# Performance work log

Hardware: AMD Instinct MI355X
Metric: run time of the kernel (lower is better)

The kernel has to match this reference:

```python
import jax, jax.numpy as jnp
import numpy as np

B, S, C = 512, 512, 32
H, L, P = 512, 2, 96


def _init(key, shape, scale=0.1):
    return jax.random.uniform(key, shape, jnp.float32, -scale, scale)


def setup_inputs() -> dict:
    key = jax.random.key(0)
    ks = jax.random.split(key, 10)
    return {
        "x": jax.random.normal(ks[0], (B, S, C), jnp.float32),
        "Wi0": _init(ks[1], (3 * H, C)),
        "Wh0": _init(ks[2], (3 * H, H)),
        "b0": _init(ks[3], (3 * H,)),
        "Wi1": _init(ks[4], (3 * H, H)),
        "Wh1": _init(ks[5], (3 * H, H)),
        "b1": _init(ks[6], (3 * H,)),
        "Wp": _init(ks[7], (P * C, H)),
        "bp": _init(ks[8], (P * C,)),
    }


def _gru_cell(xt, h, Wi, Wh, b):
    # xt: (B, in), h: (B, H). Gates stacked [r; z; n].
    gi = xt @ Wi.T + b                       # (B, 3H), fused input-side GEMM
    gir, giz, gin = jnp.split(gi, 3, axis=-1)
    Whr, Whz, Whn = jnp.split(Wh, 3, axis=0)
    r = jax.nn.sigmoid(gir + h @ Whr.T)
    z = jax.nn.sigmoid(giz + h @ Whz.T)
    # NOTE: source parses as (r * h) @ W_hn.T (reset BEFORE matmul)
    n = jnp.tanh(gin + (r * h) @ Whn.T)
    return (1.0 - z) * n + z * h


def reference(x, Wi0, Wh0, b0, Wi1, Wh1, b1, Wp, bp):
    batch = x.shape[0]
    h0 = jnp.zeros((batch, H), x.dtype)
    h1 = jnp.zeros((batch, H), x.dtype)

    def step(carry, xt):
        h0, h1 = carry
        h0 = _gru_cell(xt, h0, Wi0, Wh0, b0)
        h1 = _gru_cell(h0, h1, Wi1, Wh1, b1)
        return (h0, h1), None

    xs = jnp.swapaxes(x, 0, 1)               # (S, B, C)
    (h0, h1), _ = jax.lax.scan(step, (h0, h1), xs)
    pred = h1 @ Wp.T + bp                    # (B, P*C)
    return pred.reshape(batch, P, C)
```

## Files before the change

kernel.cpp:

```cpp
#include <hip/hip_runtime.h>
#include <cstdint>
#include <cstddef>


typedef _Float16 f16;
typedef _Float16 half8 __attribute__((ext_vector_type(8)));
typedef float f32x4 __attribute__((ext_vector_type(4)));
typedef unsigned long long u64;

#define NT 256
#define NBLK 256
#define SEQ 512
#define SC 2048.0f
#define INV_SC (1.0f / 2048.0f)
#define MFMA16(a, b, c) __builtin_amdgcn_mfma_f32_16x16x32_f16(a, b, c, 0, 0, 0)

constexpr size_t OFF_WH0H = 0;
constexpr size_t OFF_WH0L = 1572864;
constexpr size_t OFF_WI1H = 3145728;
constexpr size_t OFF_WI1L = 4718592;
constexpr size_t OFF_WH1H = 6291456;
constexpr size_t OFF_WH1L = 7864320;
constexpr size_t OFF_WPH  = 9437184;
constexpr size_t OFF_WI0H = 12582912;
constexpr size_t OFF_WI0L = 12681216;
constexpr size_t OFF_H0H  = 12779520;
constexpr size_t OFF_H0L  = 13303808;
constexpr size_t OFF_H1H0 = 13828096;
constexpr size_t OFF_H1L0 = 14352384;
constexpr size_t OFF_H1H1 = 14876672;
constexpr size_t OFF_H1L1 = 15400960;
constexpr size_t OFF_RH0  = 15925248;
constexpr size_t OFF_RH1  = 16449536;
constexpr size_t OFF_Z0   = 16973824;
constexpr size_t OFF_Z1   = 17498112;
constexpr size_t OFF_GIN  = 18022400;
constexpr size_t OFF_BAR  = 19070976;

constexpr int LO_BA   = 0;
constexpr int LO_BB   = 65536;
constexpr int LO_WXA  = 98304;
constexpr int LO_WXB  = 103424;
constexpr int LO_STG0 = 106496;
constexpr int LO_STG1 = 126976;
constexpr int LDS_BYTES = 147456;

__device__ __forceinline__ float sigm(float v) { return 1.f / (1.f + __expf(-v)); }
__device__ __forceinline__ float tanh_f(float v) { float e = __expf(2.f * v); return 1.f - 2.f / (e + 1.f); }
__device__ __forceinline__ void split2(float v, f16& hi, f16& lo) {
  f16 h = (f16)v; hi = h; lo = (f16)((v - (float)h) * SC);
}
__device__ __forceinline__ void st16(f16* p, f16 v) {
  union { f16 f; unsigned short u; } cv; cv.f = v;
  __hip_atomic_store((unsigned short*)p, cv.u, __ATOMIC_RELAXED, __HIP_MEMORY_SCOPE_AGENT);
}
__device__ __forceinline__ void st32(float* p, float v) {
  __hip_atomic_store(p, v, __ATOMIC_RELAXED, __HIP_MEMORY_SCOPE_AGENT);
}
__device__ __forceinline__ float ld16f(const f16* p) {
  unsigned short u = __hip_atomic_load((const unsigned short*)p, __ATOMIC_RELAXED, __HIP_MEMORY_SCOPE_AGENT);
  union { unsigned short u; f16 f; } cv; cv.u = u; return (float)cv.f;
}
__device__ __forceinline__ float ld32f(const float* p) {
  return __hip_atomic_load(p, __ATOMIC_RELAXED, __HIP_MEMORY_SCOPE_AGENT);
}
__device__ __forceinline__ void ld16a(const f16* p, uint4& v) {
  const u64* q = (const u64*)p;
  u64 a = __hip_atomic_load(q,     __ATOMIC_RELAXED, __HIP_MEMORY_SCOPE_AGENT);
  u64 b = __hip_atomic_load(q + 1, __ATOMIC_RELAXED, __HIP_MEMORY_SCOPE_AGENT);
  v.x = (unsigned)a; v.y = (unsigned)(a >> 32);
  v.z = (unsigned)b; v.w = (unsigned)(b >> 32);
}

__device__ __forceinline__ void ldB512(char* dst, int row0, const f16* __restrict__ src,
                                       int srcRow0, int nrows, int tid) {
  for (int idx = tid; idx < nrows * 64; idx += NT) {
    int r = idx >> 6, g = idx & 63;
    uint4 v = *(const uint4*)(src + (size_t)(srcRow0 + r) * 512 + g * 8);
    int row = row0 + r;
    *(uint4*)(dst + ((row * 1024 + g * 16) ^ ((row & 7) << 4))) = v;
  }
}
__device__ __forceinline__ void ldWX(char* wx, int row0, const f16* __restrict__ src,
                                     int srcRow0, int nrows, int tid) {
  for (int idx = tid; idx < nrows * 4; idx += NT) {
    int r = idx >> 2, g = idx & 3;
    uint4 v = *(const uint4*)(src + (size_t)(srcRow0 + r) * 32 + g * 8);
    *(uint4*)(wx + (row0 + r) * 80 + g * 16) = v;
  }
}

template<int FM>
__device__ __forceinline__ void runA(const f16* __restrict__ src, int m0, char* lds,
                                     int wm, int rowH, int rowL,
                                     int tid, int lr, int lkb,
                                     f32x4 (&am)[FM], f32x4 (&ac)[FM]) {
  char* S0 = lds + LO_STG0; char* S1 = lds + LO_STG1;
  const char* BA = lds + LO_BA;
  uint4 r0[4], r1[4], r2[4], r3[4];
  auto ld = [&](int c, uint4 (&v)[4]) {
#pragma unroll
    for (int j = 0; j < 4; ++j) { int idx = tid + j * NT; int r = idx >> 2, g = idx & 3;
      ld16a(src + (size_t)(m0 + r) * 512 + c * 32 + g * 8, v[j]); } };
  auto st = [&](char* S, uint4 (&v)[4]) {
#pragma unroll
    for (int j = 0; j < 4; ++j) { int idx = tid + j * NT; int r = idx >> 2, g = idx & 3;
      *(uint4*)(S + r * 80 + g * 16) = v[j]; } };
  auto mm = [&](const char* S, int c) {
    int rh = rowH + lr, rl = rowL + lr;
    half8 bh = *(const half8*)(BA + ((rh * 1024 + c * 64 + lkb) ^ ((rh & 7) << 4)));
    half8 bl = *(const half8*)(BA + ((rl * 1024 + c * 64 + lkb) ^ ((rl & 7) << 4)));
#pragma unroll
    for (int fm = 0; fm < FM; ++fm) {
      half8 a = *(const half8*)(S + (wm + fm * 16 + lr) * 80 + lkb);
      am[fm] = MFMA16(a, bh, am[fm]); ac[fm] = MFMA16(a, bl, ac[fm]); } };
  ld(0, r0); ld(1, r1); ld(2, r2); ld(3, r3);
  st(S0, r0);
  __syncthreads();
#pragma unroll 1
  for (int c0 = 0; c0 < 16; c0 += 4) {
    if (c0 + 4 < 16) ld(c0 + 4, r0);
    mm(S0, c0);     st(S1, r1); __syncthreads();
    if (c0 + 5 < 16) ld(c0 + 5, r1);
    mm(S1, c0 + 1); st(S0, r2); __syncthreads();
    if (c0 + 6 < 16) ld(c0 + 6, r2);
    mm(S0, c0 + 2); st(S1, r3); __syncthreads();
    if (c0 + 7 < 16) ld(c0 + 7, r3);
    mm(S1, c0 + 3); st(S0, r0); __syncthreads();
  }
}

__device__ __forceinline__ void runA1(const f16* __restrict__ s0p, const f16* __restrict__ s1p,
                                      int m0, char* lds, int wm,
                                      int tid, int lr, int lkb,
                                      f32x4 (&am)[4], f32x4 (&ac)[4]) {
  char* S0 = lds + LO_STG0; char* S1 = lds + LO_STG1;
  const char* BA = lds + LO_BA;
  uint4 r0[4], r1[4], r2[4], r3[4];
  auto ld = [&](int c, uint4 (&v)[4]) {
    const f16* s = (c < 16) ? s0p : s1p; int k0 = (c & 15) * 32;
#pragma unroll
    for (int j = 0; j < 4; ++j) { int idx = tid + j * NT; int r = idx >> 2, g = idx & 3;
      ld16a(s + (size_t)(m0 + r) * 512 + k0 + g * 8, v[j]); } };
  auto st = [&](char* S, uint4 (&v)[4]) {
#pragma unroll
    for (int j = 0; j < 4; ++j) { int idx = tid + j * NT; int r = idx >> 2, g = idx & 3;
      *(uint4*)(S + r * 80 + g * 16) = v[j]; } };
  auto mm = [&](const char* S, int c) {
    int rb = (c < 16) ? 0 : 32; int kB = (c & 15) * 64;
    int rh = rb + lr, rl = rb + 16 + lr;
    half8 bh = *(const half8*)(BA + ((rh * 1024 + kB + lkb) ^ ((rh & 7) << 4)));
    half8 bl = *(const half8*)(BA + ((rl * 1024 + kB + lkb) ^ ((rl & 7) << 4)));
#pragma unroll
    for (int fm = 0; fm < 4; ++fm) {
      half8 a = *(const half8*)(S + (wm + fm * 16 + lr) * 80 + lkb);
      am[fm] = MFMA16(a, bh, am[fm]); ac[fm] = MFMA16(a, bl, ac[fm]); } };
  ld(0, r0); ld(1, r1); ld(2, r2); ld(3, r3);
  st(S0, r0);
  __syncthreads();
#pragma unroll 1
  for (int c0 = 0; c0 < 32; c0 += 4) {
    if (c0 + 4 < 32) ld(c0 + 4, r0);
    mm(S0, c0);     st(S1, r1); __syncthreads();
    if (c0 + 5 < 32) ld(c0 + 5, r1);
    mm(S1, c0 + 1); st(S0, r2); __syncthreads();
    if (c0 + 6 < 32) ld(c0 + 6, r2);
    mm(S0, c0 + 2); st(S1, r3); __syncthreads();
    if (c0 + 7 < 32) ld(c0 + 7, r3);
    mm(S1, c0 + 3); st(S0, r0); __syncthreads();
  }
}

template<int FM>
__device__ __forceinline__ void runB(const f16* __restrict__ src, int m0, char* lds,
                                     int wm, int tid, int lr, int lkb,
                                     f32x4 (&am)[FM], f32x4 (&ac)[FM]) {
  char* S0 = lds + LO_STG0; char* S1 = lds + LO_STG1;
  const char* BB = lds + LO_BB;
  uint4 r0[4], r1[4], r2[4], r3[4];
  auto ld = [&](int c, uint4 (&v)[4]) {
#pragma unroll
    for (int j = 0; j < 4; ++j) { int idx = tid + j * NT; int r = idx >> 3, g = idx & 7;
      ld16a(src + (size_t)(m0 + r) * 512 + c * 64 + g * 8, v[j]); } };
  auto st = [&](char* S, uint4 (&v)[4]) {
#pragma unroll
    for (int j = 0; j < 4; ++j) { int idx = tid + j * NT; int r = idx >> 3, g = idx & 7;
      *(uint4*)(S + r * 144 + g * 16) = v[j]; } };
  auto mm = [&](const char* S, int c) {
#pragma unroll
    for (int ki = 0; ki < 2; ++ki) {
      int rh = lr, rl = 16 + lr;
      half8 bh = *(const half8*)(BB + ((rh * 1024 + c * 128 + ki * 64 + lkb) ^ ((rh & 7) << 4)));
      half8 bl = *(const half8*)(BB + ((rl * 1024 + c * 128 + ki * 64 + lkb) ^ ((rl & 7) << 4)));
#pragma unroll
      for (int fm = 0; fm < FM; ++fm) {
        half8 a = *(const half8*)(S + (wm + fm * 16 + lr) * 144 + ki * 64 + lkb);
        am[fm] = MFMA16(a, bh, am[fm]); ac[fm] = MFMA16(a, bl, ac[fm]); } } };
  ld(0, r0); ld(1, r1); ld(2, r2); ld(3, r3);
  st(S0, r0);
  __syncthreads();
#pragma unroll 1
  for (int c0 = 0; c0 < 8; c0 += 4) {
    if (c0 + 4 < 8) ld(c0 + 4, r0);
    mm(S0, c0);     st(S1, r1); __syncthreads();
    if (c0 + 5 < 8) ld(c0 + 5, r1);
    mm(S1, c0 + 1); st(S0, r2); __syncthreads();
    if (c0 + 6 < 8) ld(c0 + 6, r2);
    mm(S0, c0 + 2); st(S1, r3); __syncthreads();
    if (c0 + 7 < 8) ld(c0 + 7, r3);
    mm(S1, c0 + 3); st(S0, r0); __syncthreads();
  }
}

template<int FM>
__device__ __forceinline__ void mmX(const char* S0, const char* S1, const char* wx,
                                    int wm, int rowH, int rowL, int lr, int lkb,
                                    f32x4 (&am)[FM], f32x4 (&ac)[FM]) {
  half8 bh = *(const half8*)(wx + (rowH + lr) * 80 + lkb);
  half8 bl = *(const half8*)(wx + (rowL + lr) * 80 + lkb);
#pragma unroll
  for (int fm = 0; fm < FM; ++fm) {
    half8 axh = *(const half8*)(S0 + (wm + fm * 16 + lr) * 80 + lkb);
    half8 axl = *(const half8*)(S1 + (wm + fm * 16 + lr) * 80 + lkb);
    am[fm] = MFMA16(axh, bh, am[fm]);
    ac[fm] = MFMA16(axh, bl, ac[fm]);
    ac[fm] = MFMA16(axl, bh, ac[fm]);
  }
}

__device__ __forceinline__ void gbar(unsigned* bar, int bid, int tid, unsigned lg) {
  __syncthreads();
  if (bid == 0) {
    if (tid == 0) {
      __threadfence();
    } else {
      while (__hip_atomic_load(bar + tid * 16, __ATOMIC_RELAXED, __HIP_MEMORY_SCOPE_AGENT) < lg)
        __builtin_amdgcn_s_sleep(1);
    }
    __syncthreads();
    if (tid < 16)
      __hip_atomic_store(bar + 4096 + tid * 16, lg, __ATOMIC_RELAXED, __HIP_MEMORY_SCOPE_AGENT);
  } else if (tid == 0) {
    __threadfence();
    __hip_atomic_store(bar + bid * 16, lg, __ATOMIC_RELAXED, __HIP_MEMORY_SCOPE_AGENT);
  }
  if (tid == 0) {
    while (__hip_atomic_load(bar + 4096 + (bid & 15) * 16, __ATOMIC_RELAXED, __HIP_MEMORY_SCOPE_AGENT) < lg)
      __builtin_amdgcn_s_sleep(1);
  }
  __syncthreads();
}

__global__ void gru_setup(const float* __restrict__ Wi0, const float* __restrict__ Wh0,
                          const float* __restrict__ Wi1, const float* __restrict__ Wh1,
                          const float* __restrict__ Wp, char* __restrict__ ws) {
  size_t t = (size_t)blockIdx.x * blockDim.x + threadIdx.x;
  size_t st = (size_t)gridDim.x * blockDim.x;
  f16* wh0h = (f16*)(ws + OFF_WH0H); f16* wh0l = (f16*)(ws + OFF_WH0L);
  f16* wi1h = (f16*)(ws + OFF_WI1H); f16* wi1l = (f16*)(ws + OFF_WI1L);
  f16* wh1h = (f16*)(ws + OFF_WH1H); f16* wh1l = (f16*)(ws + OFF_WH1L);
  f16* wph  = (f16*)(ws + OFF_WPH);
  f16* wi0h = (f16*)(ws + OFF_WI0H); f16* wi0l = (f16*)(ws + OFF_WI0L);
  for (size_t j = t; j < (size_t)1536 * 512; j += st) {
    split2(Wh0[j], wh0h[j], wh0l[j]);
    split2(Wi1[j], wi1h[j], wi1l[j]);
    split2(Wh1[j], wh1h[j], wh1l[j]);
  }
  for (size_t j = t; j < (size_t)3072 * 512; j += st) wph[j] = (f16)Wp[j];
  for (size_t j = t; j < (size_t)1536 * 32; j += st) split2(Wi0[j], wi0h[j], wi0l[j]);
  f16* mir = (f16*)(ws + OFF_H0H);
  for (size_t j = t; j < (size_t)512 * 512 * 10; j += st) mir[j] = (f16)0.f;
  unsigned* bar = (unsigned*)(ws + OFF_BAR);
  for (size_t j = t; j < 8192; j += st) bar[j] = 0u;
}

__global__ __launch_bounds__(NT, 1) void gru_main(
    const float* __restrict__ x, const float* __restrict__ b0, const float* __restrict__ b1,
    const float* __restrict__ bp, float* __restrict__ out, char* __restrict__ ws)
{
  extern __shared__ char lds[];

  const f16* WH0Hp = (const f16*)(ws + OFF_WH0H); const f16* WH0Lp = (const f16*)(ws + OFF_WH0L);
  const f16* WI1Hp = (const f16*)(ws + OFF_WI1H); const f16* WI1Lp = (const f16*)(ws + OFF_WI1L);
  const f16* WH1Hp = (const f16*)(ws + OFF_WH1H); const f16* WH1Lp = (const f16*)(ws + OFF_WH1L);
  const f16* WPHp  = (const f16*)(ws + OFF_WPH);
  const f16* WI0Hp = (const f16*)(ws + OFF_WI0H); const f16* WI0Lp = (const f16*)(ws + OFF_WI0L);
  f16* H0H = (f16*)(ws + OFF_H0H);
  f16* H0L = (f16*)(ws + OFF_H0L);
  f16* RH0 = (f16*)(ws + OFF_RH0);
  f16* RH1 = (f16*)(ws + OFF_RH1);
  f16* Z0  = (f16*)(ws + OFF_Z0);
  f16* Z1  = (f16*)(ws + OFF_Z1);
  float* GIN = (float*)(ws + OFF_GIN);
  unsigned* bar = (unsigned*)(ws + OFF_BAR);

  const int bid = blockIdx.x, tid = threadIdx.x;
  const int wid = tid >> 6, lane = tid & 63;
  const int lr = lane & 15, lh = lane >> 4, lkb = lh << 4;
  const int xcd = bid & 7, kk = bid >> 3;

  const bool hasA = kk < 28;
  const int aid = xcd * 28 + kk;
  const int mgA = hasA ? aid / 112 : 0;
  const int sA = hasA ? aid % 112 : 0;
  const int typeA = sA < 32 ? 0 : (sA < 96 ? 1 : 2);
  const int slotA = typeA == 0 ? sA : (typeA == 1 ? sA - 32 : sA - 96);
  const int m0A = mgA * 256;
  const int wm02 = (wid >> 1) * 128, wn02 = (wid & 1) * 16;
  const int wm1 = wid * 64;

  const int pb = xcd * 32 + kk;
  const int mgB = pb >> 6, sB = pb & 63;
  const bool isN0 = sB < 32;
  const int colB0 = (sB & 31) * 16;
  const int m0B = mgB * 128, wmB = wid * 32;

  char* WXA = lds + LO_WXA; char* WXB = lds + LO_WXB;
  char* S0 = lds + LO_STG0; char* S1 = lds + LO_STG1;
  char* BA = lds + LO_BA; char* BB = lds + LO_BB;

  if (hasA) {
    if (typeA == 0) {
      ldB512(BA, 0, WH0Hp, slotA * 32, 32, tid); ldB512(BA, 32, WH0Lp, slotA * 32, 32, tid);
      ldWX(WXA, 0, WI0Hp, slotA * 32, 32, tid);  ldWX(WXA, 32, WI0Lp, slotA * 32, 32, tid);
    } else if (typeA == 1) {
      ldB512(BA, 0, WI1Hp, slotA * 16, 16, tid); ldB512(BA, 16, WI1Lp, slotA * 16, 16, tid);
      ldB512(BA, 32, WH1Hp, slotA * 16, 16, tid); ldB512(BA, 48, WH1Lp, slotA * 16, 16, tid);
    } else {
      ldB512(BA, 0, WI1Hp, 1024 + slotA * 32, 32, tid); ldB512(BA, 32, WI1Lp, 1024 + slotA * 32, 32, tid);
    }
  }
  if (isN0) {
    ldB512(BB, 0, WH0Hp, 1024 + colB0, 16, tid); ldB512(BB, 16, WH0Lp, 1024 + colB0, 16, tid);
    ldWX(WXB, 0, WI0Hp, 1024 + colB0, 16, tid);  ldWX(WXB, 16, WI0Lp, 1024 + colB0, 16, tid);
  } else {
    ldB512(BB, 0, WH1Hp, 1024 + colB0, 16, tid); ldB512(BB, 16, WH1Lp, 1024 + colB0, 16, tid);
  }
  __syncthreads();

  float biasA = 0.f;
  if (hasA) {
    if (typeA == 0)      biasA = b0[slotA * 32 + wn02 + lr];
    else if (typeA == 1) biasA = b1[slotA * 16 + lr];
    else                 biasA = b1[1024 + slotA * 32 + wn02 + lr];
  }
  const float biasB = isN0 ? b0[1024 + colB0 + lr] : 0.f;

  unsigned lg = 0;
  for (int i = 0; i <= SEQ; ++i) {
    const int wpar = i & 1;
    const f16* H1Hr = (const f16*)(ws + (wpar ? OFF_H1H0 : OFF_H1H1));
    const f16* H1Lr = (const f16*)(ws + (wpar ? OFF_H1L0 : OFF_H1L1));
    f16* H1Hw = (f16*)(ws + (wpar ? OFF_H1H1 : OFF_H1H0));
    f16* H1Lw = (f16*)(ws + (wpar ? OFF_H1L1 : OFF_H1L0));

    if (hasA) {
      if (typeA == 0 && i < SEQ) {
        float4 xr[8];
#pragma unroll
        for (int j = 0; j < 4; ++j) { int idx = tid + j * NT; int r = idx >> 2, g = idx & 3;
          const float* sx = x + (((size_t)(m0A + r)) << 14) + (size_t)i * 32 + g * 8;
          xr[2 * j] = ((const float4*)sx)[0]; xr[2 * j + 1] = ((const float4*)sx)[1]; }
        f32x4 am[8] = {}, ac[8] = {};
        runA<8>(H0H, m0A, lds, wm02, wn02, 32 + wn02, tid, lr, lkb, am, ac);
#pragma unroll
        for (int j = 0; j < 4; ++j) { int idx = tid + j * NT; int r = idx >> 2, g = idx & 3;
          union { uint4 u; f16 e[8]; } H, L;
          const float* f0 = (const float*)&xr[2 * j];
          const float* f1 = (const float*)&xr[2 * j + 1];
#pragma unroll
          for (int e = 0; e < 4; ++e) { split2(f0[e], H.e[e], L.e[e]); split2(f1[e], H.e[4 + e], L.e[4 + e]); }
          *(uint4*)(S0 + r * 80 + g * 16) = H.u; *(uint4*)(S1 + r * 80 + g * 16) = L.u; }
        __syncthreads();
        mmX<8>(S0, S1, WXA, wm02, wn02, 32 + wn02, lr, lkb, am, ac);
        const bool isR = (slotA < 16);
        const int ncol = slotA * 32 + wn02 + lr;
        size_t base = (size_t)(m0A + wm02 + lh * 4) * 512 + ncol;
#pragma unroll
        for (int fm = 0; fm < 8; ++fm)
#pragma unroll
        for (int r4 = 0; r4 < 4; ++r4) {
          size_t off = base + (size_t)(fm * 16 + r4) * 512;
          float s = sigm(am[fm][r4] + ac[fm][r4] * INV_SC + biasA);
          if (isR) {
            float h0v = ld16f(H0H + off) + ld16f(H0L + off) * INV_SC;
            st16(RH0 + off, (f16)(s * h0v));
          } else {
            st16(Z0 + off - 512, (f16)s);
          }
        }
      } else if (typeA == 1 && i >= 1) {
        f32x4 am[4] = {}, ac[4] = {};
        runA1(H0H, H1Hr, m0A, lds, wm1, tid, lr, lkb, am, ac);
        const bool isR = (slotA < 32);
        const int ncol = slotA * 16 + lr;
        size_t base = (size_t)(m0A + wm1 + lh * 4) * 512 + ncol;
#pragma unroll
        for (int fm = 0; fm < 4; ++fm)
#pragma unroll
        for (int r4 = 0; r4 < 4; ++r4) {
          size_t off = base + (size_t)(fm * 16 + r4) * 512;
          float s = sigm(am[fm][r4] + ac[fm][r4] * INV_SC + biasA);
          if (isR) {
            float h1v = ld16f(H1Hr + off) + ld16f(H1Lr + off) * INV_SC;
            st16(RH1 + off, (f16)(s * h1v));
          } else {
            st16(Z1 + off - 512, (f16)s);
          }
        }
      } else if (typeA == 2 && i >= 1) {
        f32x4 am[8] = {}, ac[8] = {};
        runA<8>(H0H, m0A, lds, wm02, wn02, 32 + wn02, tid, lr, lkb, am, ac);
        const int ncol = slotA * 32 + wn02 + lr;
        size_t base = (size_t)(m0A + wm02 + lh * 4) * 512 + ncol;
#pragma unroll
        for (int fm = 0; fm < 8; ++fm)
#pragma unroll
        for (int r4 = 0; r4 < 4; ++r4) {
          size_t off = base + (size_t)(fm * 16 + r4) * 512;
          st32(GIN + off, am[fm][r4] + ac[fm][r4] * INV_SC + biasA);
        }
      }
    }
    ++lg; gbar(bar, bid, tid, lg);

    if (isN0 ? (i < SEQ) : (i >= 1)) {
      f32x4 am[2] = {}, ac[2] = {};
      if (isN0) {
        float4 xr[4];
#pragma unroll
        for (int j = 0; j < 2; ++j) { int idx = tid + j * NT; int r = idx >> 2, g = idx & 3;
          const float* sx = x + (((size_t)(m0B + r)) << 14) + (size_t)i * 32 + g * 8;
          xr[2 * j] = ((const float4*)sx)[0]; xr[2 * j + 1] = ((const float4*)sx)[1]; }
        runB<2>(RH0, m0B, lds, wmB, tid, lr, lkb, am, ac);
#pragma unroll
        for (int j = 0; j < 2; ++j) { int idx = tid + j * NT; int r = idx >> 2, g = idx & 3;
          union { uint4 u; f16 e[8]; } H, L;
          const float* f0 = (const float*)&xr[2 * j];
          const float* f1 = (const float*)&xr[2 * j + 1];
#pragma unroll
          for (int e = 0; e < 4; ++e) { split2(f0[e], H.e[e], L.e[e]); split2(f1[e], H.e[4 + e], L.e[4 + e]); }
          *(uint4*)(S0 + r * 80 + g * 16) = H.u; *(uint4*)(S1 + r * 80 + g * 16) = L.u; }
        __syncthreads();
        mmX<2>(S0, S1, WXB, wmB, 0, 16, lr, lkb, am, ac);
        size_t base = (size_t)(m0B + wmB + lh * 4) * 512 + colB0 + lr;
#pragma unroll
        for (int fm = 0; fm < 2; ++fm)
#pragma unroll
        for (int r4 = 0; r4 < 4; ++r4) {
          size_t off = base + (size_t)(fm * 16 + r4) * 512;
          float nv = tanh_f(am[fm][r4] + ac[fm][r4] * INV_SC + biasB);
          float z = ld16f(Z0 + off);
          float h0v = ld16f(H0H + off) + ld16f(H0L + off) * INV_SC;
          float hn = (1.f - z) * nv + z * h0v;
          f16 hi, lo; split2(hn, hi, lo);
          st16(H0H + off, hi); st16(H0L + off, lo);
        }
      } else {
        runB<2>(RH1, m0B, lds, wmB, tid, lr, lkb, am, ac);
        size_t base = (size_t)(m0B + wmB + lh * 4) * 512 + colB0 + lr;
#pragma unroll
        for (int fm = 0; fm < 2; ++fm)
#pragma unroll
        for (int r4 = 0; r4 < 4; ++r4) {
          size_t off = base + (size_t)(fm * 16 + r4) * 512;
          float nv = tanh_f(am[fm][r4] + ac[fm][r4] * INV_SC + ld32f(GIN + off));
          float z = ld16f(Z1 + off);
          float h1v = ld16f(H1Hr + off) + ld16f(H1Lr + off) * INV_SC;
          float hn = (1.f - z) * nv + z * h1v;
          f16 hi, lo; split2(hn, hi, lo);
          st16(H1Hw + off, hi); st16(H1Lw + off, lo);
        }
      }
    }
    ++lg; gbar(bar, bid, tid, lg);
  }

  {
    const f16* H1p = (const f16*)(ws + OFF_H1H0);
    const int m0 = (bid >> 6) * 128, col0 = (bid & 63) * 48;
    const int wm = wid * 32;
    f32x4 acc[2][3] = {};
#pragma unroll 1
    for (int c = 0; c < 8; ++c) {
      uint4 va[4]; uint4 vb[2];
#pragma unroll
      for (int j = 0; j < 4; ++j) { int idx = tid + j * NT; int r = idx >> 3, g = idx & 7;
        va[j] = *(const uint4*)(H1p + (size_t)(m0 + r) * 512 + c * 64 + g * 8); }
#pragma unroll
      for (int j = 0; j < 2; ++j) { int idx = tid + j * NT;
        if (idx < 384) { int r = idx >> 3, g = idx & 7;
          vb[j] = *(const uint4*)(WPHp + (size_t)(col0 + r) * 512 + c * 64 + g * 8); } }
      __syncthreads();
#pragma unroll
      for (int j = 0; j < 4; ++j) { int idx = tid + j * NT; int r = idx >> 3, g = idx & 7;
        *(uint4*)(S0 + r * 144 + g * 16) = va[j]; }
#pragma unroll
      for (int j = 0; j < 2; ++j) { int idx = tid + j * NT;
        if (idx < 384) { int r = idx >> 3, g = idx & 7;
          *(uint4*)(S1 + r * 144 + g * 16) = vb[j]; } }
      __syncthreads();
#pragma unroll
      for (int ki = 0; ki < 2; ++ki) {
        half8 b[3];
#pragma unroll
        for (int fn = 0; fn < 3; ++fn)
          b[fn] = *(const half8*)(S1 + (fn * 16 + lr) * 144 + ki * 64 + lkb);
#pragma unroll
        for (int fm = 0; fm < 2; ++fm) {
          half8 a = *(const half8*)(S0 + (wm + fm * 16 + lr) * 144 + ki * 64 + lkb);
#pragma unroll
          for (int fn = 0; fn < 3; ++fn) acc[fm][fn] = MFMA16(a, b[fn], acc[fm][fn]);
        }
      }
    }
#pragma unroll
    for (int fm = 0; fm < 2; ++fm)
#pragma unroll
    for (int fn = 0; fn < 3; ++fn)
#pragma unroll
    for (int r4 = 0; r4 < 4; ++r4) {
      int m = m0 + wm + fm * 16 + lh * 4 + r4;
      int nc = col0 + fn * 16 + lr;
      out[(size_t)m * 3072 + nc] = acc[fm][fn][r4] + bp[nc];
    }
  }
}

extern "C" void kernel_launch(void* const* d_in, const int* in_sizes, int n_in,
                              void* d_out, int out_size, void* d_ws, size_t ws_size,
                              hipStream_t stream) {
  (void)in_sizes; (void)n_in; (void)out_size; (void)ws_size;
  const float* x   = (const float*)d_in[0];
  const float* Wi0 = (const float*)d_in[1];
  const float* Wh0 = (const float*)d_in[2];
  const float* b0  = (const float*)d_in[3];
  const float* Wi1 = (const float*)d_in[4];
  const float* Wh1 = (const float*)d_in[5];
  const float* b1  = (const float*)d_in[6];
  const float* Wp  = (const float*)d_in[7];
  const float* bp  = (const float*)d_in[8];
  char* ws = (char*)d_ws;
  static_assert(LDS_BYTES <= 163840, "LDS budget");
  (void)hipFuncSetAttribute(reinterpret_cast<const void*>(gru_main),
                            hipFuncAttributeMaxDynamicSharedMemorySize, LDS_BYTES);
  hipLaunchKernelGGL(gru_setup, dim3(512), dim3(NT), 0, stream, Wi0, Wh0, Wi1, Wh1, Wp, ws);
  hipLaunchKernelGGL(gru_main, dim3(NBLK), dim3(NT), LDS_BYTES, stream,
                     x, b0, b1, bp, (float*)d_out, ws);
}
```

Before: 32.78 ms.

## Use larger K-chunks with a single LDS staging buffer in recurrent GEMMs

The two alternating LDS staging buffers are replaced by one larger buffer. Each K-chunk doubles in size (64 instead of 32 for runA/runA1, 128 instead of 64 for runB), and register prefetch runs two chunks ahead. This halves the number of chunk iterations and so cuts per-chunk overhead, but each chunk now needs two barriers (after compute and after store) and more registers for prefetch. The x-input hi/lo split is staged in the same buffer in two phases, which adds extra barriers.

```diff
diff --git a/kernel.cpp b/kernel.cpp
--- a/kernel.cpp
+++ b/kernel.cpp
@@ -41,8 +41,7 @@
 constexpr int LO_BB   = 65536;
 constexpr int LO_WXA  = 98304;
 constexpr int LO_WXB  = 103424;
-constexpr int LO_STG0 = 106496;
-constexpr int LO_STG1 = 126976;
+constexpr int LO_MAIN = 106496;
 constexpr int LDS_BYTES = 147456;
 
 __device__ __forceinline__ float sigm(float v) { return 1.f / (1.f + __expf(-v)); }
@@ -95,38 +94,36 @@
                                      int wm, int rowH, int rowL,
                                      int tid, int lr, int lkb,
                                      f32x4 (&am)[FM], f32x4 (&ac)[FM]) {
-  char* S0 = lds + LO_STG0; char* S1 = lds + LO_STG1;
+  char* S = lds + LO_MAIN;
   const char* BA = lds + LO_BA;
-  uint4 r0[4], r1[4], r2[4], r3[4];
-  auto ld = [&](int c, uint4 (&v)[4]) {
-#pragma unroll
-    for (int j = 0; j < 4; ++j) { int idx = tid + j * NT; int r = idx >> 2, g = idx & 3;
-      ld16a(src + (size_t)(m0 + r) * 512 + c * 32 + g * 8, v[j]); } };
-  auto st = [&](char* S, uint4 (&v)[4]) {
-#pragma unroll
-    for (int j = 0; j < 4; ++j) { int idx = tid + j * NT; int r = idx >> 2, g = idx & 3;
-      *(uint4*)(S + r * 80 + g * 16) = v[j]; } };
-  auto mm = [&](const char* S, int c) {
-    int rh = rowH + lr, rl = rowL + lr;
-    half8 bh = *(const half8*)(BA + ((rh * 1024 + c * 64 + lkb) ^ ((rh & 7) << 4)));
-    half8 bl = *(const half8*)(BA + ((rl * 1024 + c * 64 + lkb) ^ ((rl & 7) << 4)));
-#pragma unroll
-    for (int fm = 0; fm < FM; ++fm) {
-      half8 a = *(const half8*)(S + (wm + fm * 16 + lr) * 80 + lkb);
-      am[fm] = MFMA16(a, bh, am[fm]); ac[fm] = MFMA16(a, bl, ac[fm]); } };
-  ld(0, r0); ld(1, r1); ld(2, r2); ld(3, r3);
-  st(S0, r0);
-  __syncthreads();
+  uint4 rA[8], rB[8];
+  auto ld = [&](int c, uint4 (&v)[8]) {
+    int k0 = c * 64;
+#pragma unroll
+    for (int j = 0; j < 8; ++j) { int idx = tid + j * NT; int r = idx >> 3, g = idx & 7;
+      ld16a(src + (size_t)(m0 + r) * 512 + k0 + g * 8, v[j]); } };
+  auto st = [&](uint4 (&v)[8]) {
+#pragma unroll
+    for (int j = 0; j < 8; ++j) { int idx = tid + j * NT; int r = idx >> 3, g = idx & 7;
+      *(uint4*)(S + r * 144 + g * 16) = v[j]; } };
+  auto mm = [&](int c) {
+#pragma unroll
+    for (int ki = 0; ki < 2; ++ki) {
+      int rh = rowH + lr, rl = rowL + lr;
+      half8 bh = *(const half8*)(BA + ((rh * 1024 + c * 128 + ki * 64 + lkb) ^ ((rh & 7) << 4)));
+      half8 bl = *(const half8*)(BA + ((rl * 1024 + c * 128 + ki * 64 + lkb) ^ ((rl & 7) << 4)));
+#pragma unroll
+      for (int fm = 0; fm < FM; ++fm) {
+        half8 a = *(const half8*)(S + (wm + fm * 16 + lr) * 144 + ki * 64 + lkb);
+        am[fm] = MFMA16(a, bh, am[fm]); ac[fm] = MFMA16(a, bl, ac[fm]); } } };
+  ld(0, rA); ld(1, rB);
+  st(rA); __syncthreads();
 #pragma unroll 1
-  for (int c0 = 0; c0 < 16; c0 += 4) {
-    if (c0 + 4 < 16) ld(c0 + 4, r0);
-    mm(S0, c0);     st(S1, r1); __syncthreads();
-    if (c0 + 5 < 16) ld(c0 + 5, r1);
-    mm(S1, c0 + 1); st(S0, r2); __syncthreads();
-    if (c0 + 6 < 16) ld(c0 + 6, r2);
-    mm(S0, c0 + 2); st(S1, r3); __syncthreads();
-    if (c0 + 7 < 16) ld(c0 + 7, r3);
-    mm(S1, c0 + 3); st(S0, r0); __syncthreads();
+  for (int c = 0; c < 8; ++c) {
+    if (c + 2 < 8) ld(c + 2, ((c & 1) == 0) ? rA : rB);
+    mm(c);
+    __syncthreads();
+    if (c + 1 < 8) { st(((c & 1) == 0) ? rB : rA); __syncthreads(); }
   }
 }
 
@@ -134,40 +131,37 @@
                                       int m0, char* lds, int wm,
                                       int tid, int lr, int lkb,
                                       f32x4 (&am)[4], f32x4 (&ac)[4]) {
-  char* S0 = lds + LO_STG0; char* S1 = lds + LO_STG1;
+  char* S = lds + LO_MAIN;
   const char* BA = lds + LO_BA;
-  uint4 r0[4], r1[4], r2[4], r3[4];
-  auto ld = [&](int c, uint4 (&v)[4]) {
-    const f16* s = (c < 16) ? s0p : s1p; int k0 = (c & 15) * 32;
-#pragma unroll
-    for (int j = 0; j < 4; ++j) { int idx = tid + j * NT; int r = idx >> 2, g = idx & 3;
+  uint4 rA[8], rB[8];
+  auto ld = [&](int c, uint4 (&v)[8]) {
+    const f16* s = (c < 8) ? s0p : s1p; int k0 = (c & 7) * 64;
+#pragma unroll
+    for (int j = 0; j < 8; ++j) { int idx = tid + j * NT; int r = idx >> 3, g = idx & 7;
       ld16a(s + (size_t)(m0 + r) * 512 + k0 + g * 8, v[j]); } };
-  auto st = [&](char* S, uint4 (&v)[4]) {
-#pragma unroll
-    for (int j = 0; j < 4; ++j) { int idx = tid + j * NT; int r = idx >> 2, g = idx & 3;
-      *(uint4*)(S + r * 80 + g * 16) = v[j]; } };
-  auto mm = [&](const char* S, int c) {
-    int rb = (c < 16) ? 0 : 32; int kB = (c & 15) * 64;
-    int rh = rb + lr, rl = rb + 16 + lr;
-    half8 bh = *(const half8*)(BA + ((rh * 1024 + kB + lkb) ^ ((rh & 7) << 4)));
-    half8 bl = *(const half8*)(BA + ((rl * 1024 + kB + lkb) ^ ((rl & 7) << 4)));
-#pragma unroll
-    for (int fm = 0; fm < 4; ++fm) {
-      half8 a = *(const half8*)(S + (wm + fm * 16 + lr) * 80 + lkb);
-      am[fm] = MFMA16(a, bh, am[fm]); ac[fm] = MFMA16(a, bl, ac[fm]); } };
-  ld(0, r0); ld(1, r1); ld(2, r2); ld(3, r3);
-  st(S0, r0);
-  __syncthreads();
+  auto st = [&](uint4 (&v)[8]) {
+#pragma unroll
+    for (int j = 0; j < 8; ++j) { int idx = tid + j * NT; int r = idx >> 3, g = idx & 7;
+      *(uint4*)(S + r * 144 + g * 16) = v[j]; } };
+  auto mm = [&](int c) {
+    int rb = (c < 8) ? 0 : 32; int kB = (c & 7) * 128;
+#pragma unroll
+    for (int ki = 0; ki < 2; ++ki) {
+      int rh = rb + lr, rl = rb + 16 + lr;
+      half8 bh = *(const half8*)(BA + ((rh * 1024 + kB + ki * 64 + lkb) ^ ((rh & 7) << 4)));
+      half8 bl = *(const half8*)(BA + ((rl * 1024 + kB + ki * 64 + lkb) ^ ((rl & 7) << 4)));
+#pragma unroll
+      for (int fm = 0; fm < 4; ++fm) {
+        half8 a = *(const half8*)(S + (wm + fm * 16 + lr) * 144 + ki * 64 + lkb);
+        am[fm] = MFMA16(a, bh, am[fm]); ac[fm] = MFMA16(a, bl, ac[fm]); } } };
+  ld(0, rA); ld(1, rB);
+  st(rA); __syncthreads();
 #pragma unroll 1
-  for (int c0 = 0; c0 < 32; c0 += 4) {
-    if (c0 + 4 < 32) ld(c0 + 4, r0);
-    mm(S0, c0);     st(S1, r1); __syncthreads();
-    if (c0 + 5 < 32) ld(c0 + 5, r1);
-    mm(S1, c0 + 1); st(S0, r2); __syncthreads();
-    if (c0 + 6 < 32) ld(c0 + 6, r2);
-    mm(S0, c0 + 2); st(S1, r3); __syncthreads();
-    if (c0 + 7 < 32) ld(c0 + 7, r3);
-    mm(S1, c0 + 3); st(S0, r0); __syncthreads();
+  for (int c = 0; c < 16; ++c) {
+    if (c + 2 < 16) ld(c + 2, ((c & 1) == 0) ? rA : rB);
+    mm(c);
+    __syncthreads();
+    if (c + 1 < 16) { st(((c & 1) == 0) ? rB : rA); __syncthreads(); }
   }
 }
 
@@ -175,56 +169,60 @@
 __device__ __forceinline__ void runB(const f16* __restrict__ src, int m0, char* lds,
                                      int wm, int tid, int lr, int lkb,
                                      f32x4 (&am)[FM], f32x4 (&ac)[FM]) {
-  char* S0 = lds + LO_STG0; char* S1 = lds + LO_STG1;
+  char* S = lds + LO_MAIN;
   const char* BB = lds + LO_BB;
-  uint4 r0[4], r1[4], r2[4], r3[4];
-  auto ld = [&](int c, uint4 (&v)[4]) {
-#pragma unroll
-    for (int j = 0; j < 4; ++j) { int idx = tid + j * NT; int r = idx >> 3, g = idx & 7;
-      ld16a(src + (size_t)(m0 + r) * 512 + c * 64 + g * 8, v[j]); } };
-  auto st = [&](char* S, uint4 (&v)[4]) {
-#pragma unroll
-    for (int j = 0; j < 4; ++j) { int idx = tid + j * NT; int r = idx >> 3, g = idx & 7;
-      *(uint4*)(S + r * 144 + g * 16) = v[j]; } };
-  auto mm = [&](const char* S, int c) {
-#pragma unroll
-    for (int ki = 0; ki < 2; ++ki) {
+  uint4 rA[8], rB[8];
+  auto ld = [&](int c, uint4 (&v)[8]) {
+#pragma unroll
+    for (int j = 0; j < 8; ++j) { int idx = tid + j * NT; int r = idx >> 4, g = idx & 15;
+      ld16a(src + (size_t)(m0 + r) * 512 + c * 128 + g * 8, v[j]); } };
+  auto st = [&](uint4 (&v)[8]) {
+#pragma unroll
+    for (int j = 0; j < 8; ++j) { int idx = tid + j * NT; int r = idx >> 4, g = idx & 15;
+      *(uint4*)(S + r * 272 + g * 16) = v[j]; } };
+  auto mm = [&](int c) {
+#pragma unroll
+    for (int ki = 0; ki < 4; ++ki) {
       int rh = lr, rl = 16 + lr;
-      half8 bh = *(const half8*)(BB + ((rh * 1024 + c * 128 + ki * 64 + lkb) ^ ((rh & 7) << 4)));
-      half8 bl = *(const half8*)(BB + ((rl * 1024 + c * 128 + ki * 64 + lkb) ^ ((rl & 7) << 4)));
+      half8 bh = *(const half8*)(BB + ((rh * 1024 + c * 256 + ki * 64 + lkb) ^ ((rh & 7) << 4)));
+      half8 bl = *(const half8*)(BB + ((rl * 1024 + c * 256 + ki * 64 + lkb) ^ ((rl & 7) << 4)));
 #pragma unroll
       for (int fm = 0; fm < FM; ++fm) {
-        half8 a = *(const half8*)(S + (wm + fm * 16 + lr) * 144 + ki * 64 + lkb);
+        half8 a = *(const half8*)(S + (wm + fm * 16 + lr) * 272 + ki * 64 + lkb);
         am[fm] = MFMA16(a, bh, am[fm]); ac[fm] = MFMA16(a, bl, ac[fm]); } } };
-  ld(0, r0); ld(1, r1); ld(2, r2); ld(3, r3);
-  st(S0, r0);
-  __syncthreads();
+  ld(0, rA); ld(1, rB);
+  st(rA); __syncthreads();
 #pragma unroll 1
-  for (int c0 = 0; c0 < 8; c0 += 4) {
-    if (c0 + 4 < 8) ld(c0 + 4, r0);
-    mm(S0, c0);     st(S1, r1); __syncthreads();
-    if (c0 + 5 < 8) ld(c0 + 5, r1);
-    mm(S1, c0 + 1); st(S0, r2); __syncthreads();
-    if (c0 + 6 < 8) ld(c0 + 6, r2);
-    mm(S0, c0 + 2); st(S1, r3); __syncthreads();
-    if (c0 + 7 < 8) ld(c0 + 7, r3);
-    mm(S1, c0 + 3); st(S0, r0); __syncthreads();
+  for (int c = 0; c < 4; ++c) {
+    if (c + 2 < 4) ld(c + 2, ((c & 1) == 0) ? rA : rB);
+    mm(c);
+    __syncthreads();
+    if (c + 1 < 4) { st(((c & 1) == 0) ? rB : rA); __syncthreads(); }
   }
 }
 
 template<int FM>
-__device__ __forceinline__ void mmX(const char* S0, const char* S1, const char* wx,
-                                    int wm, int rowH, int rowL, int lr, int lkb,
-                                    f32x4 (&am)[FM], f32x4 (&ac)[FM]) {
+__device__ __forceinline__ void mmXhi(const char* S, const char* wx,
+                                      int wm, int rowH, int rowL, int lr, int lkb,
+                                      f32x4 (&am)[FM], f32x4 (&ac)[FM]) {
   half8 bh = *(const half8*)(wx + (rowH + lr) * 80 + lkb);
   half8 bl = *(const half8*)(wx + (rowL + lr) * 80 + lkb);
 #pragma unroll
   for (int fm = 0; fm < FM; ++fm) {
-    half8 axh = *(const half8*)(S0 + (wm + fm * 16 + lr) * 80 + lkb);
-    half8 axl = *(const half8*)(S1 + (wm + fm * 16 + lr) * 80 + lkb);
-    am[fm] = MFMA16(axh, bh, am[fm]);
-    ac[fm] = MFMA16(axh, bl, ac[fm]);
-    ac[fm] = MFMA16(axl, bh, ac[fm]);
+    half8 a = *(const half8*)(S + (wm + fm * 16 + lr) * 80 + lkb);
+    am[fm] = MFMA16(a, bh, am[fm]);
+    ac[fm] = MFMA16(a, bl, ac[fm]);
+  }
+}
+template<int FM>
+__device__ __forceinline__ void mmXlo(const char* S, const char* wx,
+                                      int wm, int rowH, int lr, int lkb,
+                                      f32x4 (&ac)[FM]) {
+  half8 bh = *(const half8*)(wx + (rowH + lr) * 80 + lkb);
+#pragma unroll
+  for (int fm = 0; fm < FM; ++fm) {
+    half8 a = *(const half8*)(S + (wm + fm * 16 + lr) * 80 + lkb);
+    ac[fm] = MFMA16(a, bh, ac[fm]);
   }
 }
 
@@ -316,7 +314,7 @@
   const int m0B = mgB * 128, wmB = wid * 32;
 
   char* WXA = lds + LO_WXA; char* WXB = lds + LO_WXB;
-  char* S0 = lds + LO_STG0; char* S1 = lds + LO_STG1;
+  char* SM = lds + LO_MAIN;
   char* BA = lds + LO_BA; char* BB = lds + LO_BB;
 
   if (hasA) {
@@ -363,6 +361,7 @@
           xr[2 * j] = ((const float4*)sx)[0]; xr[2 * j + 1] = ((const float4*)sx)[1]; }
         f32x4 am[8] = {}, ac[8] = {};
         runA<8>(H0H, m0A, lds, wm02, wn02, 32 + wn02, tid, lr, lkb, am, ac);
+        uint4 Lk[4];
 #pragma unroll
         for (int j = 0; j < 4; ++j) { int idx = tid + j * NT; int r = idx >> 2, g = idx & 3;
           union { uint4 u; f16 e[8]; } H, L;
@@ -370,9 +369,15 @@
           const float* f1 = (const float*)&xr[2 * j + 1];
 #pragma unroll
           for (int e = 0; e < 4; ++e) { split2(f0[e], H.e[e], L.e[e]); split2(f1[e], H.e[4 + e], L.e[4 + e]); }
-          *(uint4*)(S0 + r * 80 + g * 16) = H.u; *(uint4*)(S1 + r * 80 + g * 16) = L.u; }
+          *(uint4*)(SM + r * 80 + g * 16) = H.u; Lk[j] = L.u; }
         __syncthreads();
-        mmX<8>(S0, S1, WXA, wm02, wn02, 32 + wn02, lr, lkb, am, ac);
+        mmXhi<8>(SM, WXA, wm02, wn02, 32 + wn02, lr, lkb, am, ac);
+        __syncthreads();
+#pragma unroll
+        for (int j = 0; j < 4; ++j) { int idx = tid + j * NT; int r = idx >> 2, g = idx & 3;
+          *(uint4*)(SM + r * 80 + g * 16) = Lk[j]; }
+        __syncthreads();
+        mmXlo<8>(SM, WXA, wm02, wn02, lr, lkb, ac);
         const bool isR = (slotA < 16);
         const int ncol = slotA * 32 + wn02 + lr;
         size_t base = (size_t)(m0A + wm02 + lh * 4) * 512 + ncol;
@@ -433,6 +438,7 @@
           const float* sx = x + (((size_t)(m0B + r)) << 14) + (size_t)i * 32 + g * 8;
           xr[2 * j] = ((const float4*)sx)[0]; xr[2 * j + 1] = ((const float4*)sx)[1]; }
         runB<2>(RH0, m0B, lds, wmB, tid, lr, lkb, am, ac);
+        uint4 Lk[2];
 #pragma unroll
         for (int j = 0; j < 2; ++j) { int idx = tid + j * NT; int r = idx >> 2, g = idx & 3;
           union { uint4 u; f16 e[8]; } H, L;
@@ -440,9 +446,15 @@
           const float* f1 = (const float*)&xr[2 * j + 1];
 #pragma unroll
           for (int e = 0; e < 4; ++e) { split2(f0[e], H.e[e], L.e[e]); split2(f1[e], H.e[4 + e], L.e[4 + e]); }
-          *(uint4*)(S0 + r * 80 + g * 16) = H.u; *(uint4*)(S1 + r * 80 + g * 16) = L.u; }
+          *(uint4*)(SM + r * 80 + g * 16) = H.u; Lk[j] = L.u; }
         __syncthreads();
-        mmX<2>(S0, S1, WXB, wmB, 0, 16, lr, lkb, am, ac);
+        mmXhi<2>(SM, WXB, wmB, 0, 16, lr, lkb, am, ac);
+        __syncthreads();
+#pragma unroll
+        for (int j = 0; j < 2; ++j) { int idx = tid + j * NT; int r = idx >> 2, g = idx & 3;
+          *(uint4*)(SM + r * 80 + g * 16) = Lk[j]; }
+        __syncthreads();
+        mmXlo<2>(SM, WXB, wmB, 0, lr, lkb, ac);
         size_t base = (size_t)(m0B + wmB + lh * 4) * 512 + colB0 + lr;
 #pragma unroll
         for (int fm = 0; fm < 2; ++fm)
@@ -480,6 +492,8 @@
     const f16* H1p = (const f16*)(ws + OFF_H1H0);
     const int m0 = (bid >> 6) * 128, col0 = (bid & 63) * 48;
     const int wm = wid * 32;
+    char* S0p = lds + LO_MAIN;
+    char* S1p = lds + LO_MAIN + 18432;
     f32x4 acc[2][3] = {};
 #pragma unroll 1
     for (int c = 0; c < 8; ++c) {
@@ -494,21 +508,21 @@
       __syncthreads();
 #pragma unroll
       for (int j = 0; j < 4; ++j) { int idx = tid + j * NT; int r = idx >> 3, g = idx & 7;
-        *(uint4*)(S0 + r * 144 + g * 16) = va[j]; }
+        *(uint4*)(S0p + r * 144 + g * 16) = va[j]; }
 #pragma unroll
       for (int j = 0; j < 2; ++j) { int idx = tid + j * NT;
         if (idx < 384) { int r = idx >> 3, g = idx & 7;
-          *(uint4*)(S1 + r * 144 + g * 16) = vb[j]; } }
+          *(uint4*)(S1p + r * 144 + g * 16) = vb[j]; } }
       __syncthreads();
 #pragma unroll
       for (int ki = 0; ki < 2; ++ki) {
         half8 b[3];
 #pragma unroll
         for (int fn = 0; fn < 3; ++fn)
-          b[fn] = *(const half8*)(S1 + (fn * 16 + lr) * 144 + ki * 64 + lkb);
+          b[fn] = *(const half8*)(S1p + (fn * 16 + lr) * 144 + ki * 64 + lkb);
 #pragma unroll
         for (int fm = 0; fm < 2; ++fm) {
-          half8 a = *(const half8*)(S0 + (wm + fm * 16 + lr) * 144 + ki * 64 + lkb);
+          half8 a = *(const half8*)(S0p + (wm + fm * 16 + lr) * 144 + ki * 64 + lkb);
 #pragma unroll
           for (int fn = 0; fn < 3; ++fn) acc[fm][fn] = MFMA16(a, b[fn], acc[fm][fn]);
         }
```

Measured after the change: 62.94 ms. 1.92x slower.
